# Performance work log

Hardware: AMD Instinct MI355X
Metric: run time of the kernel (lower is better)

Reference implementation:

```python
import jax, jax.numpy as jnp
import numpy as np

# Module dims (match init_kwargs)
IN_F, OUT_F = 4096, 4096
BS = 128                       # block size
NI, NO = IN_F // BS, OUT_F // BS   # 32 input blocks, 32 output blocks
ABI = 8                        # active output blocks per input block (layout col-sum)
LOWRANK = 64
BATCH, SEQ = 4, 2048


def setup_inputs() -> dict:
    key = jax.random.key(0)
    k1, k2, k3, k4 = jax.random.split(key, 4)
    std = float(np.sqrt(2.0 / (5 * min(OUT_F, IN_F))))  # init used by the module
    x = jax.random.normal(k1, (BATCH, SEQ, IN_F), jnp.float32)
    weight = jax.random.normal(k2, (IN_F, ABI, BS), jnp.float32) * std
    lowrank_first = jax.random.normal(k3, (LOWRANK, IN_F), jnp.float32) * std
    lowrank_second = jax.random.normal(k4, (OUT_F, LOWRANK), jnp.float32) * std
    # Banded circulant block layout: input block i feeds output blocks (i + a) % NO.
    # This satisfies get_indices_from_layout's uniform row/col-sum requirement.
    i = np.arange(NI)[:, None]
    a = np.arange(ABI)[None, :]
    forward_indices = jnp.asarray((i + a) % NO, dtype=jnp.int32)  # [NI, ABI]
    return dict(x=x, weight=weight, lowrank_first=lowrank_first,
                lowrank_second=lowrank_second, forward_indices=forward_indices)


def reference(x, weight, lowrank_first, lowrank_second, forward_indices):
    """Block-sparse matmul (index/scatter variant) + fused low-rank correction."""
    batch_dims = x.shape[:-1]
    xb = x.reshape(-1, NI, BS)                 # [N, NI, BS]
    W = weight.reshape(NI, BS, ABI, BS)        # [NI, BS_in, ABI, BS_out]
    # Per-(input block, active slot) contributions: small dense GEMMs.
    contrib = jnp.einsum('nib,ibac->niac', xb, W)          # [N, NI, ABI, BS]
    flat = contrib.reshape(-1, NI * ABI, BS).swapaxes(0, 1)  # [NI*ABI, N, BS]
    # Scatter-add each contribution into its destination output block.
    out_blocks = jax.ops.segment_sum(flat, forward_indices.reshape(-1),
                                     num_segments=NO)        # [NO, N, BS]
    out = out_blocks.swapaxes(0, 1).reshape(*batch_dims, OUT_F)
    # Low-rank correction: out += (x @ lowrank_first.T) @ lowrank_second.T
    h = jnp.einsum('...i,ri->...r', x, lowrank_first)         # [..., LOWRANK]
    out = out + jnp.einsum('...r,or->...o', h, lowrank_second)
    return out
```

## Files before the change

### kernel.cpp

```cpp
#include <hip/hip_runtime.h>
#include <stdint.h>

typedef unsigned short u16;
typedef short bf16x8 __attribute__((ext_vector_type(8)));
typedef float f32x4 __attribute__((ext_vector_type(4)));

#define ABI 8
#define BSZ 128
#define INF 4096
#define OUTF 4096
#define LRK 64
#define KT2 1280
#define NST 16

__device__ __forceinline__ u16 f2bf(float f) {
    uint32_t u = __float_as_uint(f);
    u += 0x7fffu + ((u >> 16) & 1u);
    return (u16)(u >> 16);
}

__device__ __forceinline__ uint32_t pk2(float a, float b) {
    uint32_t r;
    asm("v_cvt_pk_bf16_f32 %0, %1, %2" : "=v"(r) : "v"(a), "v"(b));
    return r;
}

__device__ __forceinline__ void async16(const u16* g, u16* l) {
    __builtin_amdgcn_global_load_lds(
        (const __attribute__((address_space(1))) uint32_t*)g,
        (__attribute__((address_space(3))) uint32_t*)l, 16, 0, 0);
}

#define FENCE() asm volatile("" ::: "memory")

__global__ __launch_bounds__(512) void gm_pack(
        const float* __restrict__ W, const float* __restrict__ L1,
        const float* __restrict__ L2,
        u16* __restrict__ Wb2, u16* __restrict__ L1b) {
    __shared__ u16 tile[128 * 128];
    int bid = blockIdx.x;
    int t = threadIdx.x;
    if (bid < 256) {
        int j = bid & 7, o = bid >> 3;
        int os = o >> 1, hh = o & 1;
        int i = (o + 25 + j) & 31;
        int a = 7 - j;
        int c = t & 127, b0 = t >> 7;
        const float* src = W + ((size_t)(i * BSZ) * ABI + a) * BSZ + c;
#pragma unroll 4
        for (int p = 0; p < 32; ++p) {
            int b = p * 4 + b0;
            tile[b * 128 + (c ^ ((b & 31) << 1))] =
                f2bf(src[(size_t)b * (ABI * BSZ)]);
        }
        __syncthreads();
        int b = t & 127, c0 = t >> 7;
        u16* dst = Wb2 + ((size_t)os * 256 + hh * 128) * KT2
                 + (size_t)(hh * 128 + j * 128 + b);
#pragma unroll 4
        for (int p = 0; p < 32; ++p) {
            int cc = p * 4 + c0;
            dst[(size_t)cc * KT2] = tile[b * 128 + (cc ^ ((b & 31) << 1))];
        }
    } else if (bid < 272) {
        int o = (bid - 256) * 2 + (t >> 8);
        int os = o >> 1, hh = o & 1;
        int tt = t & 255;
        int r = tt & 63, c0 = tt >> 6;
#pragma unroll 4
        for (int p = 0; p < 32; ++p) {
            int c = p * 4 + c0;
            Wb2[((size_t)os * 256 + hh * 128 + c) * KT2 + 1152 + r] =
                f2bf(L2[((size_t)o * BSZ + c) * LRK + r]);
        }
    } else {
        int idx = ((bid - 272) * 512 + t) * 4;
        f32x4 v = *reinterpret_cast<const f32x4*>(L1 + idx);
        uint32_t lo = pk2(v[0], v[1]);
        uint32_t hi = pk2(v[2], v[3]);
        *reinterpret_cast<uint32_t*>(L1b + idx)     = lo;
        *reinterpret_cast<uint32_t*>(L1b + idx + 2) = hi;
    }
}

__global__ __launch_bounds__(256) void gm_cast(
        const float* __restrict__ x, const u16* __restrict__ L1b,
        u16* __restrict__ xb, u16* __restrict__ hb) {
    __shared__ float red[4][4][256];
    int t = threadIdx.x;
    int w = t >> 6, lane = t & 63;
    int lr = lane & 15, lk = (lane >> 4) << 3;
    int rb = blockIdx.x * 16;
    int row = rb + lr;
    f32x4 acc[4];
#pragma unroll
    for (int ni = 0; ni < 4; ++ni) acc[ni] = (f32x4){0.f, 0.f, 0.f, 0.f};
    const int k_base = w * 1024;
    for (int ks = 0; ks < 32; ++ks) {
        int k0 = k_base + ks * 32 + lk;
        const float* xp = x + (size_t)row * INF + k0;
        f32x4 x0 = *reinterpret_cast<const f32x4*>(xp);
        f32x4 x1 = *reinterpret_cast<const f32x4*>(xp + 4);
        bf16x8 af;
        af[0] = (short)f2bf(x0[0]); af[1] = (short)f2bf(x0[1]);
        af[2] = (short)f2bf(x0[2]); af[3] = (short)f2bf(x0[3]);
        af[4] = (short)f2bf(x1[0]); af[5] = (short)f2bf(x1[1]);
        af[6] = (short)f2bf(x1[2]); af[7] = (short)f2bf(x1[3]);
        *reinterpret_cast<bf16x8*>(xb + (size_t)row * INF + k0) = af;
#pragma unroll
        for (int ni = 0; ni < 4; ++ni) {
            bf16x8 bv = *reinterpret_cast<const bf16x8*>(
                L1b + (size_t)(ni * 16 + lr) * INF + k0);
            acc[ni] = __builtin_amdgcn_mfma_f32_16x16x32_bf16(af, bv, acc[ni], 0, 0, 0);
        }
    }
#pragma unroll
    for (int ni = 0; ni < 4; ++ni)
#pragma unroll
        for (int j = 0; j < 4; ++j) red[w][ni][lane * 4 + j] = acc[ni][j];
    __syncthreads();
    if (t < 64) {
#pragma unroll
        for (int ni = 0; ni < 4; ++ni)
#pragma unroll
            for (int j = 0; j < 4; ++j) {
                float s = red[0][ni][lane * 4 + j] + red[1][ni][lane * 4 + j]
                        + red[2][ni][lane * 4 + j] + red[3][ni][lane * 4 + j];
                int r_ = rb + ((lane >> 4) << 2) + j;
                int c_ = ni * 16 + (lane & 15);
                hb[(size_t)r_ * LRK + c_] = f2bf(s);
            }
    }
}

__global__ __launch_bounds__(512) void gm_gemm(
        const u16* __restrict__ xb, const u16* __restrict__ hb,
        const u16* __restrict__ Wb2, float* __restrict__ out) {
    __shared__ u16 smem[65536];
    u16* Asb = smem;
    u16* Bsb = smem + 32768;

    int os = blockIdx.x;
    int mt = blockIdx.y;
    int mbase = mt * 256;
    const u16* wb = Wb2 + (size_t)os * (256 * KT2);
    int cb0 = ((2 * os + 25) * BSZ) & (INF - 1);

    int t = threadIdx.x;
    int lane = t & 63, w = t >> 6;
    int wr = w >> 2, wc = w & 3;
    int lr = lane & 15, g4 = lane >> 4;

    int sl = t & 7, row0 = t >> 3;
    int swo = (sl ^ (row0 & 7)) << 3;
    const u16* xa  = xb + (size_t)(mbase + row0) * INF + swo;
    const u16* ha  = hb + (size_t)(mbase + row0) * LRK + swo;
    const u16* wba = wb + (size_t)row0 * KT2 + swo;
    u16* AsD = Asb + t * 8;
    u16* BsD = Bsb + t * 8;

#define STAGE_A_(Tn, SD, H) do {                                            \
    u16* d_ = AsD + (SD) * 16384 + (H) * 8192;                              \
    if ((Tn) < 18) {                                                        \
        int colT_ = (cb0 + (Tn) * 64) & (INF - 1);                          \
        async16(xa + (size_t)((H) * 128) * INF + colT_, d_);                \
        async16(xa + (size_t)((H) * 128 + 64) * INF + colT_, d_ + 4096);    \
    } else {                                                                \
        async16(ha + (H) * 128 * LRK, d_);                                  \
        async16(ha + ((H) * 128 + 64) * LRK, d_ + 4096);                    \
    }                                                                       \
} while (0)
#define STAGE_B_(Tn, SD, H) do {                                            \
    u16* d_ = BsD + (SD) * 16384 + (H) * 8192;                              \
    async16(wba + (size_t)((H) * 128) * KT2 + (Tn) * 64, d_);               \
    async16(wba + (size_t)((H) * 128 + 64) * KT2 + (Tn) * 64, d_ + 4096);   \
} while (0)

    int arow = (wr * 64 + lr) * 64;
    int brow = (wc * 32 + lr) * 64;
    int ksw0 = ((g4) ^ (lr & 7)) << 3;
    int ksw1 = ((4 + g4) ^ (lr & 7)) << 3;

    f32x4 acc[2][2][4][2];
#pragma unroll
    for (int p = 0; p < 2; ++p)
#pragma unroll
        for (int q = 0; q < 2; ++q)
#pragma unroll
            for (int m = 0; m < 4; ++m)
#pragma unroll
                for (int n = 0; n < 2; ++n) acc[p][q][m][n] = (f32x4){0,0,0,0};

    bf16x8 a0k0 = {}, a1k0 = {}, a2k0 = {}, a3k0 = {};
    bf16x8 a0k1 = {}, a1k1 = {}, a2k1 = {}, a3k1 = {};
    bf16x8 p0k0 = {}, p1k0 = {}, p0k1 = {}, p1k1 = {};
    bf16x8 q0k0 = {}, q1k0 = {}, q0k1 = {}, q1k1 = {};

#define READ_A(S, H) do {                                                    \
    const u16* Ab_ = Asb + (S) * 16384 + (H) * 8192;                         \
    a0k0 = *(const bf16x8*)(Ab_ + arow + 0 * 1024 + ksw0);                   \
    a1k0 = *(const bf16x8*)(Ab_ + arow + 1 * 1024 + ksw0);                   \
    a2k0 = *(const bf16x8*)(Ab_ + arow + 2 * 1024 + ksw0);                   \
    a3k0 = *(const bf16x8*)(Ab_ + arow + 3 * 1024 + ksw0);                   \
    a0k1 = *(const bf16x8*)(Ab_ + arow + 0 * 1024 + ksw1);                   \
    a1k1 = *(const bf16x8*)(Ab_ + arow + 1 * 1024 + ksw1);                   \
    a2k1 = *(const bf16x8*)(Ab_ + arow + 2 * 1024 + ksw1);                   \
    a3k1 = *(const bf16x8*)(Ab_ + arow + 3 * 1024 + ksw1);                   \
} while (0)
#define READ_B0(S) do {                                                      \
    const u16* Bb_ = Bsb + (S) * 16384;                                      \
    p0k0 = *(const bf16x8*)(Bb_ + brow + 0 * 1024 + ksw0);                   \
    p1k0 = *(const bf16x8*)(Bb_ + brow + 1 * 1024 + ksw0);                   \
    p0k1 = *(const bf16x8*)(Bb_ + brow + 0 * 1024 + ksw1);                   \
    p1k1 = *(const bf16x8*)(Bb_ + brow + 1 * 1024 + ksw1);                   \
} while (0)
#define READ_B1(S) do {                                                      \
    const u16* Bb_ = Bsb + (S) * 16384 + 8192;                               \
    q0k0 = *(const bf16x8*)(Bb_ + brow + 0 * 1024 + ksw0);                   \
    q1k0 = *(const bf16x8*)(Bb_ + brow + 1 * 1024 + ksw0);                   \
    q0k1 = *(const bf16x8*)(Bb_ + brow + 0 * 1024 + ksw1);                   \
    q1k1 = *(const bf16x8*)(Bb_ + brow + 1 * 1024 + ksw1);                   \
} while (0)

#define SYNC(VMC)                                                            \
    asm volatile("s_waitcnt vmcnt(" VMC ")" ::: "memory");                   \
    FENCE(); __builtin_amdgcn_s_barrier(); FENCE();

#define MFMA16Q(MH, NH, B0, B1, B2, B3)                                      \
    __builtin_amdgcn_s_setprio(1);                                           \
    acc[MH][NH][0][0] = __builtin_amdgcn_mfma_f32_16x16x32_bf16(a0k0, B0, acc[MH][NH][0][0], 0,0,0); \
    acc[MH][NH][0][1] = __builtin_amdgcn_mfma_f32_16x16x32_bf16(a0k0, B1, acc[MH][NH][0][1], 0,0,0); \
    acc[MH][NH][1][0] = __builtin_amdgcn_mfma_f32_16x16x32_bf16(a1k0, B0, acc[MH][NH][1][0], 0,0,0); \
    acc[MH][NH][1][1] = __builtin_amdgcn_mfma_f32_16x16x32_bf16(a1k0, B1, acc[MH][NH][1][1], 0,0,0); \
    acc[MH][NH][2][0] = __builtin_amdgcn_mfma_f32_16x16x32_bf16(a2k0, B0, acc[MH][NH][2][0], 0,0,0); \
    acc[MH][NH][2][1] = __builtin_amdgcn_mfma_f32_16x16x32_bf16(a2k0, B1, acc[MH][NH][2][1], 0,0,0); \
    acc[MH][NH][3][0] = __builtin_amdgcn_mfma_f32_16x16x32_bf16(a3k0, B0, acc[MH][NH][3][0], 0,0,0); \
    acc[MH][NH][3][1] = __builtin_amdgcn_mfma_f32_16x16x32_bf16(a3k0, B1, acc[MH][NH][3][1], 0,0,0); \
    acc[MH][NH][0][0] = __builtin_amdgcn_mfma_f32_16x16x32_bf16(a0k1, B2, acc[MH][NH][0][0], 0,0,0); \
    acc[MH][NH][0][1] = __builtin_amdgcn_mfma_f32_16x16x32_bf16(a0k1, B3, acc[MH][NH][0][1], 0,0,0); \
    acc[MH][NH][1][0] = __builtin_amdgcn_mfma_f32_16x16x32_bf16(a1k1, B2, acc[MH][NH][1][0], 0,0,0); \
    acc[MH][NH][1][1] = __builtin_amdgcn_mfma_f32_16x16x32_bf16(a1k1, B3, acc[MH][NH][1][1], 0,0,0); \
    acc[MH][NH][2][0] = __builtin_amdgcn_mfma_f32_16x16x32_bf16(a2k1, B2, acc[MH][NH][2][0], 0,0,0); \
    acc[MH][NH][2][1] = __builtin_amdgcn_mfma_f32_16x16x32_bf16(a2k1, B3, acc[MH][NH][2][1], 0,0,0); \
    acc[MH][NH][3][0] = __builtin_amdgcn_mfma_f32_16x16x32_bf16(a3k1, B2, acc[MH][NH][3][0], 0,0,0); \
    acc[MH][NH][3][1] = __builtin_amdgcn_mfma_f32_16x16x32_bf16(a3k1, B3, acc[MH][NH][3][1], 0,0,0); \
    __builtin_amdgcn_s_setprio(0);

#define GROUP_G(S, TN, H0, H1) do {                                          \
    READ_A(S, 0);                                                            \
    if (H0) { READ_B0(S); }                                                  \
    STAGE_B_((TN), (S) ^ 1, 0);                                              \
    SYNC("4")                                                                \
    if (H0) { MFMA16Q(0, 0, p0k0, p1k0, p0k1, p1k1) }                        \
    if (H1) { READ_B1(S); }                                                  \
    STAGE_A_((TN), (S) ^ 1, 0);                                              \
    SYNC("4")                                                                \
    if (H1) { MFMA16Q(0, 1, q0k0, q1k0, q0k1, q1k1) }                        \
    READ_A(S, 1);                                                            \
    STAGE_B_((TN), (S) ^ 1, 1);                                              \
    SYNC("4")                                                                \
    if (H1) { MFMA16Q(1, 1, q0k0, q1k0, q0k1, q1k1) }                        \
    STAGE_A_((TN), (S) ^ 1, 1);                                              \
    SYNC("4")                                                                \
    if (H0) { MFMA16Q(1, 0, p0k0, p1k0, p0k1, p1k1) }                        \
} while (0)

#define GROUP_TAIL(S) do {                                                   \
    SYNC("0")                                                                \
    READ_A(S, 0); READ_B0(S);                                                \
    MFMA16Q(0, 0, p0k0, p1k0, p0k1, p1k1)                                    \
    READ_B1(S);                                                              \
    MFMA16Q(0, 1, q0k0, q1k0, q0k1, q1k1)                                    \
    READ_A(S, 1);                                                            \
    MFMA16Q(1, 1, q0k0, q1k0, q0k1, q1k1)                                    \
    MFMA16Q(1, 0, p0k0, p1k0, p0k1, p1k1)                                    \
} while (0)

    STAGE_B_(0, 0, 0); STAGE_A_(0, 0, 0); STAGE_B_(0, 0, 1); STAGE_A_(0, 0, 1);
    SYNC("4")

    GROUP_G(0, 1, 1, 0);
    GROUP_G(1, 2, 1, 0);
#pragma unroll 1
    for (int T = 2; T < 16; T += 2) {
        GROUP_G(0, T + 1, 1, 1);
        GROUP_G(1, T + 2, 1, 1);
    }
    GROUP_G(0, 17, 0, 1);
    GROUP_G(1, 18, 0, 1);
    GROUP_TAIL(0);

    float* eb = (float*)smem;
#pragma unroll
    for (int mh = 0; mh < 2; ++mh) {
        __syncthreads();
#pragma unroll
        for (int nh = 0; nh < 2; ++nh)
#pragma unroll
            for (int m = 0; m < 4; ++m)
#pragma unroll
                for (int n = 0; n < 2; ++n)
#pragma unroll
                    for (int j = 0; j < 4; ++j) {
                        int r_ = wr * 64 + m * 16 + (g4 << 2) + j;
                        int c_ = nh * 128 + wc * 32 + n * 16 + lr;
                        eb[r_ * 256 + (((c_ >> 2) ^ ((r_ & 15) << 2)) << 2)
                           + (c_ & 3)] = acc[mh][nh][m][n][j];
                    }
        __syncthreads();
#pragma unroll
        for (int pq = 0; pq < 16; ++pq) {
            int p = pq & 3, q = pq >> 2;
            int r_ = (t >> 4) + q * 32;
            int g = (t & 15) + p * 16;
            f32x4 v = *(const f32x4*)&eb[r_ * 256
                        + ((g ^ ((r_ & 15) << 2)) << 2)];
            *(f32x4*)&out[(size_t)(mbase + mh * 128 + r_) * OUTF
                          + os * 256 + g * 4] = v;
        }
    }
#undef STAGE_A_
#undef STAGE_B_
#undef READ_A
#undef READ_B0
#undef READ_B1
#undef SYNC
#undef MFMA16Q
#undef GROUP_G
#undef GROUP_TAIL
}

extern "C" void kernel_launch(void* const* d_in, const int* in_sizes, int n_in,
                              void* d_out, int out_size, void* d_ws, size_t ws_size,
                              hipStream_t stream) {
    const float* x  = (const float*)d_in[0];
    const float* W  = (const float*)d_in[1];
    const float* L1 = (const float*)d_in[2];
    const float* L2 = (const float*)d_in[3];
    float* out = (float*)d_out;

    char* ws = (char*)d_ws;
    u16* xb  = (u16*)(ws);
    u16* hb  = (u16*)(ws + 67108864);
    u16* Wb2 = (u16*)(ws + 68157440);
    u16* L1b = (u16*)(ws + 81264640);

    gm_pack<<<dim3(400), dim3(512), 0, stream>>>(W, L1, L2, Wb2, L1b);
    gm_cast<<<dim3(512), dim3(256), 0, stream>>>(x, L1b, xb, hb);
    gm_gemm<<<dim3(16, 32), dim3(512), 0, stream>>>(xb, hb, Wb2, out);
}
```

Baseline: 160.9 us.

## Restructure main GEMM loop into two phases with fewer barriers per k-step

Regroups each k-step of the MFMA main loop from four staged sub-phases, each with its own sync, into two phases. Phase one issues all B reads plus three of the four global-to-LDS stages before one sync, and phase two handles the rest. Fewer barriers and larger batches of outstanding loads are meant to cut synchronisation stalls and improve overlap. The cost is more registers held live in phase one and less interleaving of loads with MFMA.

```diff
diff --git a/kernel.cpp b/kernel.cpp
--- a/kernel.cpp
+++ b/kernel.cpp
@@ -246,30 +246,28 @@
     acc[MH][NH][3][1] = __builtin_amdgcn_mfma_f32_16x16x32_bf16(a3k1, B3, acc[MH][NH][3][1], 0,0,0); \
     __builtin_amdgcn_s_setprio(0);
 
-#define GROUP_G(S, TN, H0, H1) do {                                          \
+#define GPH1(S, TN, H0, H1) do {                                             \
     READ_A(S, 0);                                                            \
     if (H0) { READ_B0(S); }                                                  \
+    if (H1) { READ_B1(S); }                                                  \
     STAGE_B_((TN), (S) ^ 1, 0);                                              \
-    SYNC("4")                                                                \
+    STAGE_A_((TN), (S) ^ 1, 0);                                              \
+    STAGE_B_((TN), (S) ^ 1, 1);                                              \
+    SYNC("6")                                                                \
     if (H0) { MFMA16Q(0, 0, p0k0, p1k0, p0k1, p1k1) }                        \
-    if (H1) { READ_B1(S); }                                                  \
-    STAGE_A_((TN), (S) ^ 1, 0);                                              \
-    SYNC("4")                                                                \
     if (H1) { MFMA16Q(0, 1, q0k0, q1k0, q0k1, q1k1) }                        \
+} while (0)
+#define GPH2(S, TN, H0, H1) do {                                             \
     READ_A(S, 1);                                                            \
-    STAGE_B_((TN), (S) ^ 1, 1);                                              \
-    SYNC("4")                                                                \
+    STAGE_A_((TN), (S) ^ 1, 1);                                              \
+    SYNC("2")                                                                \
     if (H1) { MFMA16Q(1, 1, q0k0, q1k0, q0k1, q1k1) }                        \
-    STAGE_A_((TN), (S) ^ 1, 1);                                              \
-    SYNC("4")                                                                \
     if (H0) { MFMA16Q(1, 0, p0k0, p1k0, p0k1, p1k1) }                        \
 } while (0)
-
-#define GROUP_TAIL(S) do {                                                   \
+#define GPH1L(S) do {                                                        \
     SYNC("0")                                                                \
-    READ_A(S, 0); READ_B0(S);                                                \
+    READ_A(S, 0); READ_B0(S); READ_B1(S);                                    \
     MFMA16Q(0, 0, p0k0, p1k0, p0k1, p1k1)                                    \
-    READ_B1(S);                                                              \
     MFMA16Q(0, 1, q0k0, q1k0, q0k1, q1k1)                                    \
     READ_A(S, 1);                                                            \
     MFMA16Q(1, 1, q0k0, q1k0, q0k1, q1k1)                                    \
@@ -277,18 +275,18 @@
 } while (0)
 
     STAGE_B_(0, 0, 0); STAGE_A_(0, 0, 0); STAGE_B_(0, 0, 1); STAGE_A_(0, 0, 1);
-    SYNC("4")
-
-    GROUP_G(0, 1, 1, 0);
-    GROUP_G(1, 2, 1, 0);
+    SYNC("2")
+
+    GPH1(0, 1, 1, 0); GPH2(0, 1, 1, 0);
+    GPH1(1, 2, 1, 0); GPH2(1, 2, 1, 0);
 #pragma unroll 1
     for (int T = 2; T < 16; T += 2) {
-        GROUP_G(0, T + 1, 1, 1);
-        GROUP_G(1, T + 2, 1, 1);
-    }
-    GROUP_G(0, 17, 0, 1);
-    GROUP_G(1, 18, 0, 1);
-    GROUP_TAIL(0);
+        GPH1(0, T + 1, 1, 1); GPH2(0, T + 1, 1, 1);
+        GPH1(1, T + 2, 1, 1); GPH2(1, T + 2, 1, 1);
+    }
+    GPH1(0, 17, 0, 1); GPH2(0, 17, 0, 1);
+    GPH1(1, 18, 0, 1); GPH2(1, 18, 0, 1);
+    GPH1L(0);
 
     float* eb = (float*)smem;
 #pragma unroll
@@ -326,8 +324,9 @@
 #undef READ_B1
 #undef SYNC
 #undef MFMA16Q
-#undef GROUP_G
-#undef GROUP_TAIL
+#undef GPH1
+#undef GPH2
+#undef GPH1L
 }
 
 extern "C" void kernel_launch(void* const* d_in, const int* in_sizes, int n_in,
```

New measurement: 165.1 us. 1.03x slower.
